# Kernel optimization log

Measured on AMD Instinct MI355X. Metric: run time of the kernel, lower is better.

## Reference

```python
import jax, jax.numpy as jnp
import numpy as np

SUB_NO = 20
N_SYN = 2000
SYN_T = 201
HIST_T = 100
SYN_B = 2
HIST_B = 3
X_T = 10000


def _make_structure():
    # C_den[k] = parent(k)+1, 0 for root. Binary-ish tree over 20 subunits.
    C_den = np.zeros(SUB_NO, np.int32)
    for k in range(1, SUB_NO):
        C_den[k] = (k - 1) // 2 + 1
    # C_syn: synapse j -> subunit j%SUB_NO, sign -1 if j%5==0 else +1
    j = np.arange(N_SYN)
    sign = np.where(j % 5 == 0, -1, 1).astype(np.int32)
    C_syn = np.zeros((SUB_NO, N_SYN), np.int32)
    C_syn[j % SUB_NO, j] = sign
    return jnp.asarray(C_syn), jnp.asarray(C_den)


def setup_inputs() -> dict:
    key = jax.random.key(0)
    X = jax.random.uniform(key, (X_T, N_SYN), jnp.float32)
    C_syn, C_den = _make_structure()
    K_syn = jnp.stack([jnp.full((SUB_NO, SYN_B), 0.04, jnp.float32),
                       jnp.full((SUB_NO, SYN_B), -0.02, jnp.float32)], axis=-1)
    return {
        'X': X,
        'V_o': jnp.full((1,), -69.0, jnp.float32),
        'K_syn': K_syn,                                   # [S, Sb, 2]
        'syn_basis_tau': 1.6 + jnp.arange(SYN_B, dtype=jnp.float32),
        'Delta': jnp.full((1,), 2.0, jnp.float32),
        'C': jnp.ones((SUB_NO,), jnp.float32),
        'Theta': jnp.zeros((SUB_NO,), jnp.float32),
        'thresh': jnp.full((SUB_NO,), 85.0, jnp.float32),
        'thresh_scale': jnp.full((SUB_NO,), 100.0, jnp.float32),
        'spike_size': jnp.full((SUB_NO,), 4.0, jnp.float32),
        'hist_basis_tau': 1.7 + 0.5 * jnp.arange(HIST_B, dtype=jnp.float32),
        'K_hist': jnp.full((SUB_NO, HIST_B), 0.025, jnp.float32),
        'C_syn': C_syn,                                   # int32 [S, n_syn]
        'C_den': C_den,                                   # int32 [S]
    }


def reference(X, V_o, K_syn, syn_basis_tau, Delta, C, Theta, thresh,
              thresh_scale, spike_size, hist_basis_tau, K_hist, C_syn, C_den):
    dt = X.dtype
    sub_no = C_syn.shape[0]
    # ---- synaptic drive: sum over synapses commutes with linear conv ----
    Xe = X @ (C_syn == 1).astype(dt).T    # [T, S]
    Xi = X @ (C_syn == -1).astype(dt).T   # [T, S]
    delta = jnp.exp(Delta)[0]
    te = jnp.maximum(jnp.arange(SYN_T, dtype=dt) - delta, 0.0)
    taus = jnp.exp(syn_basis_tau)                       # [Sb]
    tt = te[None, :] / taus[:, None]
    basis = tt * jnp.exp(-tt)                           # [Sb, syn_T]
    e_kern = K_syn[:, :, 0] @ basis                     # [S, syn_T]
    i_kern = K_syn[:, :, 1] @ basis
    pad = SYN_T // 2

    def gconv(sig, kern):  # per-subunit (grouped) cross-correlation, as torch conv1d
        out = jax.lax.conv_general_dilated(
            sig.T[None], kern[:, None, :], (1,), [(pad, pad)],
            feature_group_count=sub_no)
        return out[0].T                                 # [T, S]

    subunit_in = gconv(Xe, e_kern) + gconv(Xi, i_kern)  # [T, S]

    # ---- spike-history kernels ----
    th = jnp.arange(HIST_T, dtype=dt)
    htt = th[None, :] / jnp.exp(hist_basis_tau)[:, None]
    hkerns = K_hist @ (htt * jnp.exp(-htt))             # [S, hist_T]

    expC = jnp.exp(C)
    C_den_np = np.asarray(jax.device_get(C_den))
    children = [np.where(C_den_np == s + 1)[0] for s in range(sub_no)]

    outs = [None] * sub_no
    for s in range(sub_no - 1, -1, -1):  # leaves -> root
        sub_in = subunit_in[:, s]
        for k in children[s]:
            sub_in = sub_in + outs[int(k)]
        kern, theta = hkerns[s], Theta[s]
        scale, thr, size = thresh_scale[s], thresh[s], spike_size[s]

        def step(hist, x_t):
            pre = x_t + jnp.dot(kern, hist)
            post = jax.nn.sigmoid(pre - theta)
            spk = jax.nn.sigmoid(post * scale - thr)
            hist = jnp.concatenate([spk[None], hist[:-1]])
            return hist, post + spk * size

        _, y = jax.lax.scan(step, jnp.zeros((HIST_T,), dt), sub_in)
        outs[s] = y * expC[s]
    return outs[0] + V_o[0]
```

## Files before the change

### kernel.cpp

```cpp
#include <hip/hip_runtime.h>


#define T_LEN   10000
#define NSYN    2000
#define SUBS    20
#define KLEN    201
#define CHUNK   16
#define NBLK    625
#define WARM    32
#define NITER   (CHUNK + WARM + 16)
#define NQUAD   (NITER / 4)
#define OUT_N0  (WARM + 16)
#define LPITCH  124

__device__ __forceinline__ float fexp2(float x) {
#if __has_builtin(__builtin_amdgcn_exp2f)
  return __builtin_amdgcn_exp2f(x);
#else
  return exp2f(x);
#endif
}
__device__ __forceinline__ float frcp(float x) {
#if __has_builtin(__builtin_amdgcn_rcpf)
  return __builtin_amdgcn_rcpf(x);
#else
  return 1.0f / x;
#endif
}
__device__ __forceinline__ float rfl(float x) {
  return __int_as_float(__builtin_amdgcn_readfirstlane(__float_as_int(x)));
}

typedef __attribute__((address_space(3))) uint32_t lds_u32;
typedef const __attribute__((address_space(1))) uint32_t g_u32;

__global__ __launch_bounds__(256) void k1_classsum(const float* __restrict__ X,
                                                   float* __restrict__ sig) {
  __shared__ __align__(16) float xrow[8192];
  const int tid = threadIdx.x;
  const int t_base = blockIdx.x * 4;
  const size_t rowbase = (size_t)t_base * 500;
  const int wave = tid >> 6, lane = tid & 63;
  const float4* Xv = (const float4*)X;
#pragma unroll
  for (int k = 0; k < 8; ++k) {
    size_t gidx = rowbase + (size_t)(tid + 256 * k);
    if (gidx > 4999999u) gidx = 4999999u;
    unsigned ldsoff = (unsigned)((wave * 64 + 256 * k) * 16);
    __builtin_amdgcn_global_load_lds(
        (g_u32*)(Xv + gidx),
        (lds_u32*)(uint32_t*)((char*)xrow + ldsoff),
        16, 0, 0);
  }
  __syncthreads();

  const float* row = xrow + wave * NSYN;
  float acc = 0.f;
  if (lane < 60) {
#pragma unroll
    for (int k = 0; k < 33; ++k) acc += row[lane + 60 * k];
  }
  if (lane < 20) acc += row[1980 + lane];
  float a1 = __shfl(acc, (lane + 20 < 64) ? lane + 20 : 63);
  float a2 = __shfl(acc, (lane + 40 < 64) ? lane + 40 : 63);
  if (lane < 20) sig[(size_t)lane * T_LEN + t_base + wave] = acc + a1 + a2;
}

__global__ __launch_bounds__(256) void k2_conv(
    const float* __restrict__ sig, const float* __restrict__ K_syn,
    const float* __restrict__ sbt, const float* __restrict__ Delta,
    float* __restrict__ subT) {
  __shared__ __align__(16) float wsig[1232];
  __shared__ __align__(16) float kern[208];
  const int tid = threadIdx.x;
  const int s = blockIdx.y;
  const int t0 = blockIdx.x * 1024;
  const float delta = __expf(Delta[0]);
  const float it0 = __expf(-sbt[0]);
  const float it1 = __expf(-sbt[1]);
  const int c = (s % 5 == 0) ? 1 : 0;
  const float ka = K_syn[s * 4 + c];
  const float kb = K_syn[s * 4 + 2 + c];
  if (tid < 208) {
    float val = 0.f;
    if (tid < KLEN) {
      float te = fmaxf((float)tid - delta, 0.f);
      float ta = te * it0, tb = te * it1;
      val = ka * (ta * __expf(-ta)) + kb * (tb * __expf(-tb));
    }
    kern[tid] = val;
  }
  const float* srow = sig + (size_t)s * T_LEN;
#pragma unroll
  for (int k = 0; k < 5; ++k) {
    int e = tid + 256 * k;
    if (e < 1232) {
      int col = t0 - 100 + e;
      wsig[e] = (e < 1224 && col >= 0 && col < T_LEN) ? srow[col] : 0.f;
    }
  }
  __syncthreads();

  const float4* wv = (const float4*)wsig;
  float4 qA = wv[tid], qB = wv[tid + 1];
  float a0 = 0.f, a1 = 0.f, a2 = 0.f, a3 = 0.f;
#pragma unroll
  for (int g = 0; g < 51; ++g) {
    float4 kv = *(const float4*)&kern[4 * g];
    float4 qC = wv[tid + g + 2];
    a0 = fmaf(kv.x, qA.x, fmaf(kv.y, qA.y, fmaf(kv.z, qA.z, fmaf(kv.w, qA.w, a0))));
    a1 = fmaf(kv.x, qA.y, fmaf(kv.y, qA.z, fmaf(kv.z, qA.w, fmaf(kv.w, qB.x, a1))));
    a2 = fmaf(kv.x, qA.z, fmaf(kv.y, qA.w, fmaf(kv.z, qB.x, fmaf(kv.w, qB.y, a2))));
    a3 = fmaf(kv.x, qA.w, fmaf(kv.y, qB.x, fmaf(kv.z, qB.y, fmaf(kv.w, qB.z, a3))));
    qA = qB; qB = qC;
  }
  int t = t0 + 4 * tid;
  if (t < T_LEN) {
    float4 o; o.x = a0; o.y = a1; o.z = a2; o.w = a3;
    *(float4*)(subT + (size_t)s * T_LEN + t) = o;
  }
}

__global__ __launch_bounds__(64) void k3_scan(
    const float* __restrict__ subT, const float* __restrict__ V_o,
    const float* __restrict__ C, const float* __restrict__ Theta,
    const float* __restrict__ thresh, const float* __restrict__ tscale,
    const float* __restrict__ ssize, const float* __restrict__ hbt,
    const float* __restrict__ K_hist, float* __restrict__ out) {
  __shared__ __align__(16) float lds_subT[SUBS * LPITCH];
  const int lane = threadIdx.x;
  const int s = (lane < SUBS) ? lane : SUBS - 1;
  const int b = blockIdx.x;
  const int t_start = b * CHUNK - WARM;
  const float Vo = V_o[0];

#pragma unroll
  for (int k = 0; k < 10; ++k) {
    int i = lane + 64 * k;
    if (i < 620) {
      int ss = i / 31, q = i - ss * 31;
      int col = t_start - 16 + 4 * q;
      col = (col < 0) ? 0 : ((col > 9996) ? 9996 : col);
      *(float4*)&lds_subT[ss * LPITCH + 4 * q] =
          *(const float4*)(subT + (size_t)ss * T_LEN + col);
    }
  }
  __syncthreads();

  const float L2E = 1.4426950408889634f;
  float eC = __expf(C[s]);
  float szC = ssize[s];
  const float thL = Theta[s] * L2E;
  const float aspk = -tscale[s] * L2E;
  const float bspk = thresh[s] * L2E;
  float k0 = K_hist[s * 3 + 0], k1 = K_hist[s * 3 + 1], k2 = K_hist[s * 3 + 2];
  if (lane >= SUBS) { eC = 0.f; k0 = 0.f; k1 = 0.f; k2 = 0.f; }
  szC *= eC;

  float rho0, rho1, rho2, rt0, rt1, rt2;
  {
    float it, rr;
    it = __expf(-hbt[0]); rr = __expf(-it); rho0 = rfl(rr); rt0 = rfl(rr * it);
    it = __expf(-hbt[1]); rr = __expf(-it); rho1 = rfl(rr); rt1 = rfl(rr * it);
    it = __expf(-hbt[2]); rr = __expf(-it); rho2 = rfl(rr); rt2 = rfl(rr * it);
  }

  const int d = 31 - __clz(s + 1);
  const int skew = 4 * (4 - d);
  const int cl = (2 * lane + 1 < 64) ? 2 * lane + 1 : 63;
  const int cr = (2 * lane + 2 < 64) ? 2 * lane + 2 : 63;
  int t = t_start - skew;

  float F0 = 0, F1 = 0, F2 = 0, G0 = 0, G1 = 0, G2 = 0;
  float pL0 = 0, pL1 = 0, pL2 = 0, pL3 = 0;
  float pR0 = 0, pR1 = 0, pR2 = 0, pR3 = 0;
  float nL0, nL1, nL2, nL3, nR0, nR1, nR2, nR3;

  const int subbase = s * LPITCH + (16 - skew);
  float4 subq = *(const float4*)&lds_subT[subbase];

#define STEP(J, SUBV, PLV, PRV)                                             \
  {                                                                         \
    float conv = fmaf(k0, F0, fmaf(k1, F1, k2 * F2));                       \
    float pre = (SUBV + conv) + (PLV + PRV);                                \
    float u = fexp2(fmaf(pre, -L2E, thL));                                  \
    float post = frcp(1.f + u);                                             \
    float v = fexp2(fmaf(post, aspk, bspk));                                \
    float spk = frcp(1.f + v);                                              \
    spk = ((t + J) < 0) ? 0.f : spk;                                        \
    F0 = fmaf(rho0, F0, rt0 * G0);                                          \
    F1 = fmaf(rho1, F1, rt1 * G1);                                          \
    F2 = fmaf(rho2, F2, rt2 * G2);                                          \
    G0 = fmaf(rho0, G0, spk);                                               \
    G1 = fmaf(rho1, G1, spk);                                               \
    G2 = fmaf(rho2, G2, spk);                                               \
    float y = fmaf(spk, szC, post * eC);                                    \
    if ((n + J) >= OUT_N0) {                                                \
      if (lane == 0) out[t + J] = y + Vo;                                   \
    }                                                                       \
    nL##J = __shfl(y, cl);                                                  \
    nR##J = __shfl(y, cr);                                                  \
  }

  for (int n4 = 0; n4 < NQUAD; ++n4) {
    const int n = n4 << 2;
    float4 subq_n = *(const float4*)&lds_subT[subbase + n + 4];
    STEP(0, subq.x, pL0, pR0)
    STEP(1, subq.y, pL1, pR1)
    STEP(2, subq.z, pL2, pR2)
    STEP(3, subq.w, pL3, pR3)
    subq = subq_n;
    pL0 = nL0; pL1 = nL1; pL2 = nL2; pL3 = nL3;
    pR0 = nR0; pR1 = nR1; pR2 = nR2; pR3 = nR3;
    t += 4;
  }
#undef STEP
}

extern "C" void kernel_launch(void* const* d_in, const int* in_sizes, int n_in,
                              void* d_out, int out_size, void* d_ws, size_t ws_size,
                              hipStream_t stream) {
  (void)in_sizes; (void)n_in; (void)out_size; (void)ws_size;
  const float* X      = (const float*)d_in[0];
  const float* V_o    = (const float*)d_in[1];
  const float* K_syn  = (const float*)d_in[2];
  const float* sbt    = (const float*)d_in[3];
  const float* Delta  = (const float*)d_in[4];
  const float* C      = (const float*)d_in[5];
  const float* Theta  = (const float*)d_in[6];
  const float* thr    = (const float*)d_in[7];
  const float* tsc    = (const float*)d_in[8];
  const float* ssz    = (const float*)d_in[9];
  const float* hbt    = (const float*)d_in[10];
  const float* K_hist = (const float*)d_in[11];
  float* out   = (float*)d_out;
  float* subT  = (float*)d_ws;
  float* sig   = (float*)((char*)d_ws + 800000);

  hipLaunchKernelGGL(k1_classsum, dim3(T_LEN / 4), dim3(256), 0, stream, X, sig);
  hipLaunchKernelGGL(k2_conv, dim3(10, 20), dim3(256), 0, stream,
                     sig, K_syn, sbt, Delta, subT);
  hipLaunchKernelGGL(k3_scan, dim3(NBLK), dim3(64), 0, stream, subT, V_o, C,
                     Theta, thr, tsc, ssz, hbt, K_hist, out);
}
```

Measured before the change: 33.85 us.

## Fuse three kernels into one persistent kernel with software grid barriers

Merges the class-sum, convolution and scan kernels into one persistent launch of 512 blocks, separated by atomic-counter grid barriers. This removes two kernel launch gaps and the inter-kernel drain. The scan stage is rechunked to 500 blocks of 20 steps with a shorter warm-up. The cost is a memset launch, barrier spin latency, and a dependence on all 512 blocks being co-resident, since otherwise the barrier can hang or time out.

```diff
diff --git a/kernel.cpp b/kernel.cpp
--- a/kernel.cpp
+++ b/kernel.cpp
@@ -5,13 +5,15 @@
 #define NSYN    2000
 #define SUBS    20
 #define KLEN    201
-#define CHUNK   16
-#define NBLK    625
-#define WARM    32
+#define NPERS   512
+#define CHUNK   20
+#define K3BLK   500
+#define WARM    24
 #define NITER   (CHUNK + WARM + 16)
 #define NQUAD   (NITER / 4)
 #define OUT_N0  (WARM + 16)
 #define LPITCH  124
+#define CTR_OFF 1600000
 
 __device__ __forceinline__ float fexp2(float x) {
 #if __has_builtin(__builtin_amdgcn_exp2f)
@@ -34,150 +36,168 @@
 typedef __attribute__((address_space(3))) uint32_t lds_u32;
 typedef const __attribute__((address_space(1))) uint32_t g_u32;
 
-__global__ __launch_bounds__(256) void k1_classsum(const float* __restrict__ X,
-                                                   float* __restrict__ sig) {
-  __shared__ __align__(16) float xrow[8192];
+__device__ __forceinline__ void gbar(unsigned* c, int bid, int tid) {
+  __syncthreads();
+  if (tid == 0) {
+    __threadfence();
+    unsigned old = __hip_atomic_fetch_add(&c[(bid >> 5) * 32], 1u,
+                                          __ATOMIC_ACQ_REL, __HIP_MEMORY_SCOPE_AGENT);
+    if (old == 31u)
+      __hip_atomic_fetch_add(&c[512], 1u, __ATOMIC_ACQ_REL, __HIP_MEMORY_SCOPE_AGENT);
+    int lim = 8000000;
+    while (__hip_atomic_load(&c[512], __ATOMIC_ACQUIRE, __HIP_MEMORY_SCOPE_AGENT) < 16u
+           && --lim)
+      __builtin_amdgcn_s_sleep(2);
+  }
+  __syncthreads();
+}
+
+__global__ __launch_bounds__(256, 2) void fused_shglm(
+    const float* __restrict__ X, const float* __restrict__ V_o,
+    const float* __restrict__ K_syn, const float* __restrict__ sbt,
+    const float* __restrict__ Delta, const float* __restrict__ C,
+    const float* __restrict__ Theta, const float* __restrict__ thresh,
+    const float* __restrict__ tscale, const float* __restrict__ ssize,
+    const float* __restrict__ hbt, const float* __restrict__ K_hist,
+    float* __restrict__ out, float* __restrict__ subT,
+    float* __restrict__ sig, unsigned* __restrict__ ctr) {
+  __shared__ __align__(16) char pool[32768];
   const int tid = threadIdx.x;
-  const int t_base = blockIdx.x * 4;
-  const size_t rowbase = (size_t)t_base * 500;
-  const int wave = tid >> 6, lane = tid & 63;
-  const float4* Xv = (const float4*)X;
-#pragma unroll
-  for (int k = 0; k < 8; ++k) {
-    size_t gidx = rowbase + (size_t)(tid + 256 * k);
-    if (gidx > 4999999u) gidx = 4999999u;
-    unsigned ldsoff = (unsigned)((wave * 64 + 256 * k) * 16);
-    __builtin_amdgcn_global_load_lds(
-        (g_u32*)(Xv + gidx),
-        (lds_u32*)(uint32_t*)((char*)xrow + ldsoff),
-        16, 0, 0);
-  }
-  __syncthreads();
-
-  const float* row = xrow + wave * NSYN;
-  float acc = 0.f;
-  if (lane < 60) {
-#pragma unroll
-    for (int k = 0; k < 33; ++k) acc += row[lane + 60 * k];
-  }
-  if (lane < 20) acc += row[1980 + lane];
-  float a1 = __shfl(acc, (lane + 20 < 64) ? lane + 20 : 63);
-  float a2 = __shfl(acc, (lane + 40 < 64) ? lane + 40 : 63);
-  if (lane < 20) sig[(size_t)lane * T_LEN + t_base + wave] = acc + a1 + a2;
-}
-
-__global__ __launch_bounds__(256) void k2_conv(
-    const float* __restrict__ sig, const float* __restrict__ K_syn,
-    const float* __restrict__ sbt, const float* __restrict__ Delta,
-    float* __restrict__ subT) {
-  __shared__ __align__(16) float wsig[1232];
-  __shared__ __align__(16) float kern[208];
-  const int tid = threadIdx.x;
-  const int s = blockIdx.y;
-  const int t0 = blockIdx.x * 1024;
-  const float delta = __expf(Delta[0]);
-  const float it0 = __expf(-sbt[0]);
-  const float it1 = __expf(-sbt[1]);
-  const int c = (s % 5 == 0) ? 1 : 0;
-  const float ka = K_syn[s * 4 + c];
-  const float kb = K_syn[s * 4 + 2 + c];
-  if (tid < 208) {
-    float val = 0.f;
-    if (tid < KLEN) {
-      float te = fmaxf((float)tid - delta, 0.f);
-      float ta = te * it0, tb = te * it1;
-      val = ka * (ta * __expf(-ta)) + kb * (tb * __expf(-tb));
-    }
-    kern[tid] = val;
-  }
-  const float* srow = sig + (size_t)s * T_LEN;
-#pragma unroll
-  for (int k = 0; k < 5; ++k) {
-    int e = tid + 256 * k;
-    if (e < 1232) {
-      int col = t0 - 100 + e;
-      wsig[e] = (e < 1224 && col >= 0 && col < T_LEN) ? srow[col] : 0.f;
-    }
-  }
-  __syncthreads();
-
-  const float4* wv = (const float4*)wsig;
-  float4 qA = wv[tid], qB = wv[tid + 1];
-  float a0 = 0.f, a1 = 0.f, a2 = 0.f, a3 = 0.f;
-#pragma unroll
-  for (int g = 0; g < 51; ++g) {
-    float4 kv = *(const float4*)&kern[4 * g];
-    float4 qC = wv[tid + g + 2];
-    a0 = fmaf(kv.x, qA.x, fmaf(kv.y, qA.y, fmaf(kv.z, qA.z, fmaf(kv.w, qA.w, a0))));
-    a1 = fmaf(kv.x, qA.y, fmaf(kv.y, qA.z, fmaf(kv.z, qA.w, fmaf(kv.w, qB.x, a1))));
-    a2 = fmaf(kv.x, qA.z, fmaf(kv.y, qA.w, fmaf(kv.z, qB.x, fmaf(kv.w, qB.y, a2))));
-    a3 = fmaf(kv.x, qA.w, fmaf(kv.y, qB.x, fmaf(kv.z, qB.y, fmaf(kv.w, qB.z, a3))));
-    qA = qB; qB = qC;
-  }
-  int t = t0 + 4 * tid;
-  if (t < T_LEN) {
-    float4 o; o.x = a0; o.y = a1; o.z = a2; o.w = a3;
-    *(float4*)(subT + (size_t)s * T_LEN + t) = o;
-  }
-}
-
-__global__ __launch_bounds__(64) void k3_scan(
-    const float* __restrict__ subT, const float* __restrict__ V_o,
-    const float* __restrict__ C, const float* __restrict__ Theta,
-    const float* __restrict__ thresh, const float* __restrict__ tscale,
-    const float* __restrict__ ssize, const float* __restrict__ hbt,
-    const float* __restrict__ K_hist, float* __restrict__ out) {
-  __shared__ __align__(16) float lds_subT[SUBS * LPITCH];
-  const int lane = threadIdx.x;
-  const int s = (lane < SUBS) ? lane : SUBS - 1;
-  const int b = blockIdx.x;
-  const int t_start = b * CHUNK - WARM;
-  const float Vo = V_o[0];
-
-#pragma unroll
-  for (int k = 0; k < 10; ++k) {
-    int i = lane + 64 * k;
-    if (i < 620) {
-      int ss = i / 31, q = i - ss * 31;
-      int col = t_start - 16 + 4 * q;
-      col = (col < 0) ? 0 : ((col > 9996) ? 9996 : col);
-      *(float4*)&lds_subT[ss * LPITCH + 4 * q] =
-          *(const float4*)(subT + (size_t)ss * T_LEN + col);
-    }
-  }
-  __syncthreads();
-
-  const float L2E = 1.4426950408889634f;
-  float eC = __expf(C[s]);
-  float szC = ssize[s];
-  const float thL = Theta[s] * L2E;
-  const float aspk = -tscale[s] * L2E;
-  const float bspk = thresh[s] * L2E;
-  float k0 = K_hist[s * 3 + 0], k1 = K_hist[s * 3 + 1], k2 = K_hist[s * 3 + 2];
-  if (lane >= SUBS) { eC = 0.f; k0 = 0.f; k1 = 0.f; k2 = 0.f; }
-  szC *= eC;
-
-  float rho0, rho1, rho2, rt0, rt1, rt2;
+  const int bid = blockIdx.x;
+
   {
-    float it, rr;
-    it = __expf(-hbt[0]); rr = __expf(-it); rho0 = rfl(rr); rt0 = rfl(rr * it);
-    it = __expf(-hbt[1]); rr = __expf(-it); rho1 = rfl(rr); rt1 = rfl(rr * it);
-    it = __expf(-hbt[2]); rr = __expf(-it); rho2 = rfl(rr); rt2 = rfl(rr * it);
-  }
-
-  const int d = 31 - __clz(s + 1);
-  const int skew = 4 * (4 - d);
-  const int cl = (2 * lane + 1 < 64) ? 2 * lane + 1 : 63;
-  const int cr = (2 * lane + 2 < 64) ? 2 * lane + 2 : 63;
-  int t = t_start - skew;
-
-  float F0 = 0, F1 = 0, F2 = 0, G0 = 0, G1 = 0, G2 = 0;
-  float pL0 = 0, pL1 = 0, pL2 = 0, pL3 = 0;
-  float pR0 = 0, pR1 = 0, pR2 = 0, pR3 = 0;
-  float nL0, nL1, nL2, nL3, nR0, nR1, nR2, nR3;
-
-  const int subbase = s * LPITCH + (16 - skew);
-  float4 subq = *(const float4*)&lds_subT[subbase];
+    float* xrow = (float*)pool;
+    const float4* Xv = (const float4*)X;
+    const int wave = tid >> 6, lane = tid & 63;
+    for (int rb = bid * 4; rb < T_LEN; rb += NPERS * 4) {
+      const size_t rowbase = (size_t)rb * 500;
+#pragma unroll
+      for (int k = 0; k < 8; ++k) {
+        size_t gidx = rowbase + (size_t)(tid + 256 * k);
+        if (gidx > 4999999u) gidx = 4999999u;
+        unsigned ldsoff = (unsigned)((wave * 64 + 256 * k) * 16);
+        __builtin_amdgcn_global_load_lds((g_u32*)(Xv + gidx),
+                                         (lds_u32*)(uint32_t*)(pool + ldsoff),
+                                         16, 0, 0);
+      }
+      __syncthreads();
+      const float* row = xrow + wave * NSYN;
+      float acc = 0.f;
+      if (lane < 60) {
+#pragma unroll
+        for (int k = 0; k < 33; ++k) acc += row[lane + 60 * k];
+      }
+      if (lane < 20) acc += row[1980 + lane];
+      float a1 = __shfl(acc, (lane + 20 < 64) ? lane + 20 : 63);
+      float a2 = __shfl(acc, (lane + 40 < 64) ? lane + 40 : 63);
+      if (lane < 20) sig[(size_t)lane * T_LEN + rb + wave] = acc + a1 + a2;
+      __syncthreads();
+    }
+  }
+
+  gbar(ctr, bid, tid);
+
+  if ((bid & 1) == 0 && bid < 400) {
+    const int item = bid >> 1;
+    const int s = item / 10;
+    const int t0 = (item - s * 10) * 1024;
+    float* wsig = (float*)pool;
+    float* kern = (float*)(pool + 4928);
+    const float delta = __expf(Delta[0]);
+    const float it0 = __expf(-sbt[0]);
+    const float it1 = __expf(-sbt[1]);
+    const int c = (s % 5 == 0) ? 1 : 0;
+    const float ka = K_syn[s * 4 + c];
+    const float kb = K_syn[s * 4 + 2 + c];
+    if (tid < 208) {
+      float val = 0.f;
+      if (tid < KLEN) {
+        float te = fmaxf((float)tid - delta, 0.f);
+        float ta = te * it0, tb = te * it1;
+        val = ka * (ta * __expf(-ta)) + kb * (tb * __expf(-tb));
+      }
+      kern[tid] = val;
+    }
+    const float* srow = sig + (size_t)s * T_LEN;
+#pragma unroll
+    for (int k = 0; k < 5; ++k) {
+      int e = tid + 256 * k;
+      if (e < 1232) {
+        int col = t0 - 100 + e;
+        wsig[e] = (e < 1224 && col >= 0 && col < T_LEN) ? srow[col] : 0.f;
+      }
+    }
+    __syncthreads();
+    const float4* wv = (const float4*)wsig;
+    float4 qA = wv[tid], qB = wv[tid + 1];
+    float a0 = 0.f, a1 = 0.f, a2 = 0.f, a3 = 0.f;
+#pragma unroll
+    for (int g = 0; g < 51; ++g) {
+      float4 kv = *(const float4*)&kern[4 * g];
+      float4 qC = wv[tid + g + 2];
+      a0 = fmaf(kv.x, qA.x, fmaf(kv.y, qA.y, fmaf(kv.z, qA.z, fmaf(kv.w, qA.w, a0))));
+      a1 = fmaf(kv.x, qA.y, fmaf(kv.y, qA.z, fmaf(kv.z, qA.w, fmaf(kv.w, qB.x, a1))));
+      a2 = fmaf(kv.x, qA.z, fmaf(kv.y, qA.w, fmaf(kv.z, qB.x, fmaf(kv.w, qB.y, a2))));
+      a3 = fmaf(kv.x, qA.w, fmaf(kv.y, qB.x, fmaf(kv.z, qB.y, fmaf(kv.w, qB.z, a3))));
+      qA = qB; qB = qC;
+    }
+    int t = t0 + 4 * tid;
+    if (t < T_LEN) {
+      float4 o; o.x = a0; o.y = a1; o.z = a2; o.w = a3;
+      *(float4*)(subT + (size_t)s * T_LEN + t) = o;
+    }
+  }
+
+  gbar(ctr + 1024, bid, tid);
+
+  if (bid < K3BLK) {
+    float* lds_subT = (float*)pool;
+    const int b = bid;
+    const int t_start = b * CHUNK - WARM;
+#pragma unroll
+    for (int k = 0; k < 3; ++k) {
+      int i = tid + 256 * k;
+      if (i < 620) {
+        int ss = i / 31, q = i - ss * 31;
+        int col = t_start - 16 + 4 * q;
+        col = (col < 0) ? 0 : ((col > 9996) ? 9996 : col);
+        *(float4*)&lds_subT[ss * LPITCH + 4 * q] =
+            *(const float4*)(subT + (size_t)ss * T_LEN + col);
+      }
+    }
+    __syncthreads();
+    if (tid < 64) {
+      const int lane = tid;
+      const int s = (lane < SUBS) ? lane : SUBS - 1;
+      const float Vo = V_o[0];
+      const float L2E = 1.4426950408889634f;
+      float eC = __expf(C[s]);
+      float szC = ssize[s];
+      const float thL = Theta[s] * L2E;
+      const float aspk = -tscale[s] * L2E;
+      const float bspk = thresh[s] * L2E;
+      float k0 = K_hist[s * 3 + 0], k1 = K_hist[s * 3 + 1], k2 = K_hist[s * 3 + 2];
+      if (lane >= SUBS) { eC = 0.f; k0 = 0.f; k1 = 0.f; k2 = 0.f; }
+      szC *= eC;
+      float rho0, rho1, rho2, rt0, rt1, rt2;
+      {
+        float it, rr;
+        it = __expf(-hbt[0]); rr = __expf(-it); rho0 = rfl(rr); rt0 = rfl(rr * it);
+        it = __expf(-hbt[1]); rr = __expf(-it); rho1 = rfl(rr); rt1 = rfl(rr * it);
+        it = __expf(-hbt[2]); rr = __expf(-it); rho2 = rfl(rr); rt2 = rfl(rr * it);
+      }
+      const int d = 31 - __clz(s + 1);
+      const int skew = 4 * (4 - d);
+      const int cl = (2 * lane + 1 < 64) ? 2 * lane + 1 : 63;
+      const int cr = (2 * lane + 2 < 64) ? 2 * lane + 2 : 63;
+      int t = t_start - skew;
+
+      float F0 = 0, F1 = 0, F2 = 0, G0 = 0, G1 = 0, G2 = 0;
+      float pL0 = 0, pL1 = 0, pL2 = 0, pL3 = 0;
+      float pR0 = 0, pR1 = 0, pR2 = 0, pR3 = 0;
+      float nL0, nL1, nL2, nL3, nR0, nR1, nR2, nR3;
+      const int subbase = s * LPITCH + (16 - skew);
+      float4 subq = *(const float4*)&lds_subT[subbase];
 
 #define STEP(J, SUBV, PLV, PRV)                                             \
   {                                                                         \
@@ -202,19 +222,21 @@
     nR##J = __shfl(y, cr);                                                  \
   }
 
-  for (int n4 = 0; n4 < NQUAD; ++n4) {
-    const int n = n4 << 2;
-    float4 subq_n = *(const float4*)&lds_subT[subbase + n + 4];
-    STEP(0, subq.x, pL0, pR0)
-    STEP(1, subq.y, pL1, pR1)
-    STEP(2, subq.z, pL2, pR2)
-    STEP(3, subq.w, pL3, pR3)
-    subq = subq_n;
-    pL0 = nL0; pL1 = nL1; pL2 = nL2; pL3 = nL3;
-    pR0 = nR0; pR1 = nR1; pR2 = nR2; pR3 = nR3;
-    t += 4;
-  }
+      for (int n4 = 0; n4 < NQUAD; ++n4) {
+        const int n = n4 << 2;
+        float4 subq_n = *(const float4*)&lds_subT[subbase + n + 4];
+        STEP(0, subq.x, pL0, pR0)
+        STEP(1, subq.y, pL1, pR1)
+        STEP(2, subq.z, pL2, pR2)
+        STEP(3, subq.w, pL3, pR3)
+        subq = subq_n;
+        pL0 = nL0; pL1 = nL1; pL2 = nL2; pL3 = nL3;
+        pR0 = nR0; pR1 = nR1; pR2 = nR2; pR3 = nR3;
+        t += 4;
+      }
 #undef STEP
+    }
+  }
 }
 
 extern "C" void kernel_launch(void* const* d_in, const int* in_sizes, int n_in,
@@ -236,10 +258,10 @@
   float* out   = (float*)d_out;
   float* subT  = (float*)d_ws;
   float* sig   = (float*)((char*)d_ws + 800000);
-
-  hipLaunchKernelGGL(k1_classsum, dim3(T_LEN / 4), dim3(256), 0, stream, X, sig);
-  hipLaunchKernelGGL(k2_conv, dim3(10, 20), dim3(256), 0, stream,
-                     sig, K_syn, sbt, Delta, subT);
-  hipLaunchKernelGGL(k3_scan, dim3(NBLK), dim3(64), 0, stream, subT, V_o, C,
-                     Theta, thr, tsc, ssz, hbt, K_hist, out);
-}
+  unsigned* ctr = (unsigned*)((char*)d_ws + CTR_OFF);
+
+  hipMemsetAsync((void*)ctr, 0, 8192, stream);
+  hipLaunchKernelGGL(fused_shglm, dim3(NPERS), dim3(256), 0, stream,
+                     X, V_o, K_syn, sbt, Delta, C, Theta, thr, tsc, ssz,
+                     hbt, K_hist, out, subT, sig, ctr);
+}
```

New measurement: 114.1 us. +237.2%, slower.

## Fuse synaptic convolution into scan kernel with per-block recomputed windows

Applied to the files above, without the earlier changes.

Merges the convolution kernel and the recurrent scan kernel into one launch. Each block loads a windowed slice of the class-summed signal for all 20 subunits, builds the kernels in LDS, convolves into LDS, then runs the 64-lane scan over a longer chunk with a shorter warm-up. This drops one launch and the global round trip of the intermediate subunit drive. In exchange each block recomputes convolution halos and kernel weights, and the scan phase leaves three of four waves idle.

```diff
diff --git a/kernel.cpp b/kernel.cpp
--- a/kernel.cpp
+++ b/kernel.cpp
@@ -5,13 +5,15 @@
 #define NSYN    2000
 #define SUBS    20
 #define KLEN    201
-#define CHUNK   16
-#define NBLK    625
-#define WARM    32
+#define CHUNK   40
+#define NBLK    250
+#define WARM    24
 #define NITER   (CHUNK + WARM + 16)
 #define NQUAD   (NITER / 4)
 #define OUT_N0  (WARM + 16)
-#define LPITCH  124
+#define LPITCH  100
+#define SGP     308
+#define KP      208
 
 __device__ __forceinline__ float fexp2(float x) {
 #if __has_builtin(__builtin_amdgcn_exp2f)
@@ -66,118 +68,108 @@
   if (lane < 20) sig[(size_t)lane * T_LEN + t_base + wave] = acc + a1 + a2;
 }
 
-__global__ __launch_bounds__(256) void k2_conv(
-    const float* __restrict__ sig, const float* __restrict__ K_syn,
-    const float* __restrict__ sbt, const float* __restrict__ Delta,
-    float* __restrict__ subT) {
-  __shared__ __align__(16) float wsig[1232];
-  __shared__ __align__(16) float kern[208];
+__global__ __launch_bounds__(256) void k23_fused(
+    const float* __restrict__ sig, const float* __restrict__ V_o,
+    const float* __restrict__ K_syn, const float* __restrict__ sbt,
+    const float* __restrict__ Delta, const float* __restrict__ C,
+    const float* __restrict__ Theta, const float* __restrict__ thresh,
+    const float* __restrict__ tscale, const float* __restrict__ ssize,
+    const float* __restrict__ hbt, const float* __restrict__ K_hist,
+    float* __restrict__ out) {
+  __shared__ __align__(16) float sigw[SUBS * SGP];
+  __shared__ __align__(16) float kern[SUBS * KP];
+  __shared__ __align__(16) float lds_subT[SUBS * LPITCH];
   const int tid = threadIdx.x;
-  const int s = blockIdx.y;
-  const int t0 = blockIdx.x * 1024;
-  const float delta = __expf(Delta[0]);
-  const float it0 = __expf(-sbt[0]);
-  const float it1 = __expf(-sbt[1]);
-  const int c = (s % 5 == 0) ? 1 : 0;
-  const float ka = K_syn[s * 4 + c];
-  const float kb = K_syn[s * 4 + 2 + c];
-  if (tid < 208) {
-    float val = 0.f;
-    if (tid < KLEN) {
-      float te = fmaxf((float)tid - delta, 0.f);
-      float ta = te * it0, tb = te * it1;
-      val = ka * (ta * __expf(-ta)) + kb * (tb * __expf(-tb));
-    }
-    kern[tid] = val;
-  }
-  const float* srow = sig + (size_t)s * T_LEN;
-#pragma unroll
-  for (int k = 0; k < 5; ++k) {
-    int e = tid + 256 * k;
-    if (e < 1232) {
-      int col = t0 - 100 + e;
-      wsig[e] = (e < 1224 && col >= 0 && col < T_LEN) ? srow[col] : 0.f;
-    }
-  }
-  __syncthreads();
-
-  const float4* wv = (const float4*)wsig;
-  float4 qA = wv[tid], qB = wv[tid + 1];
-  float a0 = 0.f, a1 = 0.f, a2 = 0.f, a3 = 0.f;
-#pragma unroll
-  for (int g = 0; g < 51; ++g) {
-    float4 kv = *(const float4*)&kern[4 * g];
-    float4 qC = wv[tid + g + 2];
-    a0 = fmaf(kv.x, qA.x, fmaf(kv.y, qA.y, fmaf(kv.z, qA.z, fmaf(kv.w, qA.w, a0))));
-    a1 = fmaf(kv.x, qA.y, fmaf(kv.y, qA.z, fmaf(kv.z, qA.w, fmaf(kv.w, qB.x, a1))));
-    a2 = fmaf(kv.x, qA.z, fmaf(kv.y, qA.w, fmaf(kv.z, qB.x, fmaf(kv.w, qB.y, a2))));
-    a3 = fmaf(kv.x, qA.w, fmaf(kv.y, qB.x, fmaf(kv.z, qB.y, fmaf(kv.w, qB.z, a3))));
-    qA = qB; qB = qC;
-  }
-  int t = t0 + 4 * tid;
-  if (t < T_LEN) {
-    float4 o; o.x = a0; o.y = a1; o.z = a2; o.w = a3;
-    *(float4*)(subT + (size_t)s * T_LEN + t) = o;
-  }
-}
-
-__global__ __launch_bounds__(64) void k3_scan(
-    const float* __restrict__ subT, const float* __restrict__ V_o,
-    const float* __restrict__ C, const float* __restrict__ Theta,
-    const float* __restrict__ thresh, const float* __restrict__ tscale,
-    const float* __restrict__ ssize, const float* __restrict__ hbt,
-    const float* __restrict__ K_hist, float* __restrict__ out) {
-  __shared__ __align__(16) float lds_subT[SUBS * LPITCH];
-  const int lane = threadIdx.x;
-  const int s = (lane < SUBS) ? lane : SUBS - 1;
   const int b = blockIdx.x;
   const int t_start = b * CHUNK - WARM;
-  const float Vo = V_o[0];
-
-#pragma unroll
-  for (int k = 0; k < 10; ++k) {
-    int i = lane + 64 * k;
-    if (i < 620) {
-      int ss = i / 31, q = i - ss * 31;
-      int col = t_start - 16 + 4 * q;
-      col = (col < 0) ? 0 : ((col > 9996) ? 9996 : col);
-      *(float4*)&lds_subT[ss * LPITCH + 4 * q] =
-          *(const float4*)(subT + (size_t)ss * T_LEN + col);
+
+  {
+    const int col0 = t_start - 116;
+    for (int i = tid; i < SUBS * 77; i += 256) {
+      int s = i / 77, f4 = i - s * 77;
+      int col = col0 + 4 * f4;
+      float4 v = {0.f, 0.f, 0.f, 0.f};
+      if (col >= 0 && col < T_LEN)
+        v = *(const float4*)(sig + (size_t)s * T_LEN + col);
+      *(float4*)&sigw[s * SGP + 4 * f4] = v;
+    }
+  }
+  {
+    const float delta = __expf(Delta[0]);
+    const float it0 = __expf(-sbt[0]);
+    const float it1 = __expf(-sbt[1]);
+    for (int i = tid; i < SUBS * KP; i += 256) {
+      int s = i / KP, k = i - s * KP;
+      float val = 0.f;
+      if (k < KLEN) {
+        int c = (s % 5 == 0) ? 1 : 0;
+        float te = fmaxf((float)k - delta, 0.f);
+        float ta = te * it0, tb = te * it1;
+        val = K_syn[s * 4 + c] * (ta * __expf(-ta)) +
+              K_syn[s * 4 + 2 + c] * (tb * __expf(-tb));
+      }
+      kern[i] = val;
     }
   }
   __syncthreads();
 
-  const float L2E = 1.4426950408889634f;
-  float eC = __expf(C[s]);
-  float szC = ssize[s];
-  const float thL = Theta[s] * L2E;
-  const float aspk = -tscale[s] * L2E;
-  const float bspk = thresh[s] * L2E;
-  float k0 = K_hist[s * 3 + 0], k1 = K_hist[s * 3 + 1], k2 = K_hist[s * 3 + 2];
-  if (lane >= SUBS) { eC = 0.f; k0 = 0.f; k1 = 0.f; k2 = 0.f; }
-  szC *= eC;
-
-  float rho0, rho1, rho2, rt0, rt1, rt2;
-  {
-    float it, rr;
-    it = __expf(-hbt[0]); rr = __expf(-it); rho0 = rfl(rr); rt0 = rfl(rr * it);
-    it = __expf(-hbt[1]); rr = __expf(-it); rho1 = rfl(rr); rt1 = rfl(rr * it);
-    it = __expf(-hbt[2]); rr = __expf(-it); rho2 = rfl(rr); rt2 = rfl(rr * it);
-  }
-
-  const int d = 31 - __clz(s + 1);
-  const int skew = 4 * (4 - d);
-  const int cl = (2 * lane + 1 < 64) ? 2 * lane + 1 : 63;
-  const int cr = (2 * lane + 2 < 64) ? 2 * lane + 2 : 63;
-  int t = t_start - skew;
-
-  float F0 = 0, F1 = 0, F2 = 0, G0 = 0, G1 = 0, G2 = 0;
-  float pL0 = 0, pL1 = 0, pL2 = 0, pL3 = 0;
-  float pR0 = 0, pR1 = 0, pR2 = 0, pR3 = 0;
-  float nL0, nL1, nL2, nL3, nR0, nR1, nR2, nR3;
-
-  const int subbase = s * LPITCH + (16 - skew);
-  float4 subq = *(const float4*)&lds_subT[subbase];
+#pragma unroll
+  for (int pass = 0; pass < 2; ++pass) {
+    int it = tid + 256 * pass;
+    if (it < 500) {
+      int s = it / 25, q = it - s * 25;
+      const float4* wvs = (const float4*)&sigw[s * SGP];
+      const float4* kern4 = (const float4*)&kern[s * KP];
+      float4 qA = wvs[q], qB = wvs[q + 1];
+      float a0 = 0.f, a1 = 0.f, a2 = 0.f, a3 = 0.f;
+#pragma unroll
+      for (int g = 0; g < 51; ++g) {
+        float4 kv = kern4[g];
+        float4 qC = wvs[q + g + 2];
+        a0 = fmaf(kv.x, qA.x, fmaf(kv.y, qA.y, fmaf(kv.z, qA.z, fmaf(kv.w, qA.w, a0))));
+        a1 = fmaf(kv.x, qA.y, fmaf(kv.y, qA.z, fmaf(kv.z, qA.w, fmaf(kv.w, qB.x, a1))));
+        a2 = fmaf(kv.x, qA.z, fmaf(kv.y, qA.w, fmaf(kv.z, qB.x, fmaf(kv.w, qB.y, a2))));
+        a3 = fmaf(kv.x, qA.w, fmaf(kv.y, qB.x, fmaf(kv.z, qB.y, fmaf(kv.w, qB.z, a3))));
+        qA = qB; qB = qC;
+      }
+      float4 o; o.x = a0; o.y = a1; o.z = a2; o.w = a3;
+      *(float4*)&lds_subT[s * LPITCH + 4 * q] = o;
+    }
+  }
+  __syncthreads();
+
+  if (tid < 64) {
+    const int lane = tid;
+    const int s = (lane < SUBS) ? lane : SUBS - 1;
+    const float Vo = V_o[0];
+    const float L2E = 1.4426950408889634f;
+    float eC = __expf(C[s]);
+    float szC = ssize[s];
+    const float thL = Theta[s] * L2E;
+    const float aspk = -tscale[s] * L2E;
+    const float bspk = thresh[s] * L2E;
+    float k0 = K_hist[s * 3 + 0], k1 = K_hist[s * 3 + 1], k2 = K_hist[s * 3 + 2];
+    if (lane >= SUBS) { eC = 0.f; k0 = 0.f; k1 = 0.f; k2 = 0.f; }
+    szC *= eC;
+    float rho0, rho1, rho2, rt0, rt1, rt2;
+    {
+      float it, rr;
+      it = __expf(-hbt[0]); rr = __expf(-it); rho0 = rfl(rr); rt0 = rfl(rr * it);
+      it = __expf(-hbt[1]); rr = __expf(-it); rho1 = rfl(rr); rt1 = rfl(rr * it);
+      it = __expf(-hbt[2]); rr = __expf(-it); rho2 = rfl(rr); rt2 = rfl(rr * it);
+    }
+    const int d = 31 - __clz(s + 1);
+    const int skew = 4 * (4 - d);
+    const int cl = (2 * lane + 1 < 64) ? 2 * lane + 1 : 63;
+    const int cr = (2 * lane + 2 < 64) ? 2 * lane + 2 : 63;
+    int t = t_start - skew;
+
+    float F0 = 0, F1 = 0, F2 = 0, G0 = 0, G1 = 0, G2 = 0;
+    float pL0 = 0, pL1 = 0, pL2 = 0, pL3 = 0;
+    float pR0 = 0, pR1 = 0, pR2 = 0, pR3 = 0;
+    float nL0, nL1, nL2, nL3, nR0, nR1, nR2, nR3;
+    const int subbase = s * LPITCH + (16 - skew);
+    float4 subq = *(const float4*)&lds_subT[subbase];
 
 #define STEP(J, SUBV, PLV, PRV)                                             \
   {                                                                         \
@@ -202,19 +194,20 @@
     nR##J = __shfl(y, cr);                                                  \
   }
 
-  for (int n4 = 0; n4 < NQUAD; ++n4) {
-    const int n = n4 << 2;
-    float4 subq_n = *(const float4*)&lds_subT[subbase + n + 4];
-    STEP(0, subq.x, pL0, pR0)
-    STEP(1, subq.y, pL1, pR1)
-    STEP(2, subq.z, pL2, pR2)
-    STEP(3, subq.w, pL3, pR3)
-    subq = subq_n;
-    pL0 = nL0; pL1 = nL1; pL2 = nL2; pL3 = nL3;
-    pR0 = nR0; pR1 = nR1; pR2 = nR2; pR3 = nR3;
-    t += 4;
-  }
+    for (int n4 = 0; n4 < NQUAD; ++n4) {
+      const int n = n4 << 2;
+      float4 subq_n = *(const float4*)&lds_subT[subbase + n + 4];
+      STEP(0, subq.x, pL0, pR0)
+      STEP(1, subq.y, pL1, pR1)
+      STEP(2, subq.z, pL2, pR2)
+      STEP(3, subq.w, pL3, pR3)
+      subq = subq_n;
+      pL0 = nL0; pL1 = nL1; pL2 = nL2; pL3 = nL3;
+      pR0 = nR0; pR1 = nR1; pR2 = nR2; pR3 = nR3;
+      t += 4;
+    }
 #undef STEP
+  }
 }
 
 extern "C" void kernel_launch(void* const* d_in, const int* in_sizes, int n_in,
@@ -233,13 +226,11 @@
   const float* ssz    = (const float*)d_in[9];
   const float* hbt    = (const float*)d_in[10];
   const float* K_hist = (const float*)d_in[11];
-  float* out   = (float*)d_out;
-  float* subT  = (float*)d_ws;
-  float* sig   = (float*)((char*)d_ws + 800000);
+  float* out = (float*)d_out;
+  float* sig = (float*)((char*)d_ws + 800000);
 
   hipLaunchKernelGGL(k1_classsum, dim3(T_LEN / 4), dim3(256), 0, stream, X, sig);
-  hipLaunchKernelGGL(k2_conv, dim3(10, 20), dim3(256), 0, stream,
-                     sig, K_syn, sbt, Delta, subT);
-  hipLaunchKernelGGL(k3_scan, dim3(NBLK), dim3(64), 0, stream, subT, V_o, C,
-                     Theta, thr, tsc, ssz, hbt, K_hist, out);
-}
+  hipLaunchKernelGGL(k23_fused, dim3(NBLK), dim3(256), 0, stream,
+                     sig, V_o, K_syn, sbt, Delta, C, Theta, thr, tsc, ssz,
+                     hbt, K_hist, out);
+}
```

Result: slower. 35.19 us (+3.9%).
